# Kernel tuning notes

Measured on AMD Instinct MI355X. Metric: run time of the kernel, lower is better.

Reference implementation:

```python
import jax, jax.numpy as jnp
import numpy as np

BETA = 0.25


def setup_inputs() -> dict:
    key = jax.random.key(0)
    k1, k2 = jax.random.split(key)
    z = jax.random.normal(k1, (16, 2048, 64), dtype=jnp.float32)
    emb = jax.random.uniform(k2, (8192, 64), dtype=jnp.float32)  # uniform_() init
    return {"z": z, "emb": emb}


def reference(z, emb):
    # z: [B, N, D], emb: [K, D]; use_norm=False so norm is identity.
    B, N, D = z.shape
    zf = z.reshape(-1, D)                                   # [B*N, D]
    # Squared euclidean distances; argmin is identical to cdist(p=2) argmin.
    d2 = (
        jnp.sum(zf * zf, axis=1, keepdims=True)
        - 2.0 * (zf @ emb.T)
        + jnp.sum(emb * emb, axis=1)
    )                                                       # [B*N, K]
    idx = jnp.argmin(d2, axis=1)                            # [B*N]
    z_q = emb[idx].reshape(z.shape)                         # [B, N, D]
    loss = BETA * jnp.mean((jax.lax.stop_gradient(z_q) - z) ** 2) + jnp.mean(
        (z_q - jax.lax.stop_gradient(z)) ** 2
    )
    z_q_st = z + jax.lax.stop_gradient(z_q - z)             # straight-through
    return z_q_st, idx, loss
```

## Files before the change

### kernel.cpp

```cpp
#include <hip/hip_runtime.h>
#include <hip/hip_bf16.h>
#include <math.h>

#define D 64
#define K_CODES 8192
#define M_QUERIES 32768
#define SLICES 4
#define CODES_PER_SLICE (K_CODES / SLICES)
#define CHUNK 64
#define NCHUNK (CODES_PER_SLICE / CHUNK)
#define QPB 128
#define TAU_V 4e-3f

typedef __attribute__((ext_vector_type(8))) short bf16x8;
typedef __attribute__((ext_vector_type(4))) float f32x4;
typedef __attribute__((ext_vector_type(16))) float f32x16;

__device__ __forceinline__ unsigned short f2bf(float x) {
    __hip_bfloat16 h = __float2bfloat16(x);
    return *reinterpret_cast<unsigned short*>(&h);
}
__device__ __forceinline__ float bf2f(unsigned short s) {
    __hip_bfloat16 h;
    *reinterpret_cast<unsigned short*>(&h) = s;
    return __bfloat162float(h);
}
__device__ __forceinline__ void gld_lds16(const void* g, void* l) {
    __builtin_amdgcn_global_load_lds(
        (const __attribute__((address_space(1))) void*)g,
        (__attribute__((address_space(3))) void*)l, 16, 0, 0);
}
__device__ __forceinline__ void gld_lds4(const void* g, void* l) {
    __builtin_amdgcn_global_load_lds(
        (const __attribute__((address_space(1))) void*)g,
        (__attribute__((address_space(3))) void*)l, 4, 0, 0);
}

__global__ __launch_bounds__(256) void k0_split(const float* __restrict__ emb,
                                                unsigned short* __restrict__ e_hi,
                                                unsigned short* __restrict__ e_lo,
                                                float* __restrict__ halfee,
                                                int* __restrict__ ws_cnt) {
    const int t = threadIdx.x;
    const int chunk = blockIdx.x;
    if (chunk == 0 && t == 0) *ws_cnt = 0;
    const int u = t & 7;
#pragma unroll
    for (int it = 0; it < 2; ++it) {
        const int r = (t >> 3) + it * 32;
        const float* src = emb + ((size_t)(chunk * 64 + r) * 64 + u * 8);
        float4 f0 = *(const float4*)(src);
        float4 f1 = *(const float4*)(src + 4);
        float f[8] = {f0.x, f0.y, f0.z, f0.w, f1.x, f1.y, f1.z, f1.w};
        bf16x8 h, lo;
        float s = 0.f;
#pragma unroll
        for (int j = 0; j < 8; ++j) {
            float e = f[j];
            s += e * e;
            unsigned short hh = f2bf(e);
            h[j]  = (short)hh;
            lo[j] = (short)f2bf(e - bf2f(hh));
        }
        size_t off = (size_t)chunk * 8192 + (size_t)(u * 64 + r) * 16;
        *(bf16x8*)((char*)e_hi + off) = h;
        *(bf16x8*)((char*)e_lo + off) = lo;
        s += __shfl_xor(s, 1);
        s += __shfl_xor(s, 2);
        s += __shfl_xor(s, 4);
        if (u == 0) halfee[chunk * 64 + r] = 0.5f * s + 128.0f;
    }
}

__global__ __launch_bounds__(256, 1) void k1_mfma(const float* __restrict__ z,
                                                  const unsigned short* __restrict__ e_hi,
                                                  const unsigned short* __restrict__ e_lo,
                                                  const float* __restrict__ halfee,
                                                  float4* __restrict__ ws_part) {
    __shared__ __align__(16) unsigned short ldshi[2][CHUNK * 64];
    __shared__ __align__(16) unsigned short ldslo[2][CHUNK * 64];
    __shared__ __align__(16) float ldshe[2][CHUNK];

    const int tid = threadIdx.x;
    const int wid = tid >> 6;
    const int l   = tid & 63;
    const int col = l & 31;
    const int hi  = l >> 5;
    const int slice = blockIdx.y;
    const int chunk0 = slice * NCHUNK;

    const int qw0 = blockIdx.x * QPB + wid * 32;
    const int qrow = qw0 + col;
    bf16x8 qh[4], ql[4];
#pragma unroll
    for (int kk = 0; kk < 4; ++kk) {
        const float* src = z + (size_t)qrow * D + kk * 16 + hi * 8;
        float4 f0 = *(const float4*)(src);
        float4 f1 = *(const float4*)(src + 4);
        float f[8] = {f0.x, f0.y, f0.z, f0.w, f1.x, f1.y, f1.z, f1.w};
        bf16x8 h, lo;
#pragma unroll
        for (int j = 0; j < 8; ++j) {
            float x = -f[j];
            unsigned short hh = f2bf(x);
            float r = x - bf2f(hh);
            h[j]  = (short)hh;
            lo[j] = (short)f2bf(r);
        }
        qh[kk] = h;
        ql[kk] = lo;
    }

    float g1 = 1e30f, g2 = 1e30f;
    int   gi = 0x7fffffff;

#define STAGE(buf, c1)                                                           \
    {                                                                            \
        size_t cb = (size_t)(chunk0 + (c1)) * 8192 + wid * 2048 + l * 16;        \
        const char* ghi = (const char*)e_hi + cb;                                \
        const char* glo = (const char*)e_lo + cb;                                \
        char* dhi = (char*)&ldshi[buf][0] + wid * 2048;                          \
        char* dlo = (char*)&ldslo[buf][0] + wid * 2048;                          \
        gld_lds16(ghi, dhi);                                                     \
        gld_lds16(ghi + 1024, dhi + 1024);                                       \
        gld_lds16(glo, dlo);                                                     \
        gld_lds16(glo + 1024, dlo + 1024);                                       \
        if (wid == 0)                                                            \
            gld_lds4((const char*)halfee + (size_t)(chunk0 + (c1)) * 256 + l * 4,\
                     (char*)&ldshe[buf][0]);                                     \
    }

#define COMPUTE(bufc, cbase)                                                     \
    {                                                                            \
        const char*  bh  = (const char*)ldshi[bufc];                             \
        const char*  bl  = (const char*)ldslo[bufc];                             \
        const float* bhe = ldshe[bufc];                                          \
        f32x16 acc0, acc1;                                                       \
        _Pragma("unroll") for (int g = 0; g < 4; ++g) {                          \
            f32x4 h0 = *(const f32x4*)(bhe + g * 8 + 4 * hi);                    \
            f32x4 h1 = *(const f32x4*)(bhe + 32 + g * 8 + 4 * hi);               \
            acc0[g * 4 + 0] = h0[0]; acc0[g * 4 + 1] = h0[1];                    \
            acc0[g * 4 + 2] = h0[2]; acc0[g * 4 + 3] = h0[3];                    \
            acc1[g * 4 + 0] = h1[0]; acc1[g * 4 + 1] = h1[1];                    \
            acc1[g * 4 + 2] = h1[2]; acc1[g * 4 + 3] = h1[3];                    \
        }                                                                        \
        _Pragma("unroll") for (int kk = 0; kk < 4; ++kk) {                       \
            int a0 = ((kk * 2 + hi) * 64 + col) * 16;       \
            bf16x8 ah0 = *(const bf16x8*)(bh + a0);                              \
            bf16x8 ah1 = *(const bf16x8*)(bh + a0 + 512);                        \
            bf16x8 al0 = *(const bf16x8*)(bl + a0);                              \
            bf16x8 al1 = *(const bf16x8*)(bl + a0 + 512);                        \
            acc0 = __builtin_amdgcn_mfma_f32_32x32x16_bf16(ah0, qh[kk], acc0, 0, 0, 0); \
            acc1 = __builtin_amdgcn_mfma_f32_32x32x16_bf16(ah1, qh[kk], acc1, 0, 0, 0); \
            acc0 = __builtin_amdgcn_mfma_f32_32x32x16_bf16(ah0, ql[kk], acc0, 0, 0, 0); \
            acc1 = __builtin_amdgcn_mfma_f32_32x32x16_bf16(ah1, ql[kk], acc1, 0, 0, 0); \
            acc0 = __builtin_amdgcn_mfma_f32_32x32x16_bf16(al0, qh[kk], acc0, 0, 0, 0); \
            acc1 = __builtin_amdgcn_mfma_f32_32x32x16_bf16(al1, qh[kk], acc1, 0, 0, 0); \
        }                                                                        \
        float m1p = 1e30f, m2p = 1e30f;                                          \
        _Pragma("unroll") for (int r = 0; r < 16; ++r) {                         \
            float vp0 = __int_as_float((__float_as_int(acc0[r]) & 0xFFFFFFE0) | r); \
            m2p = __builtin_amdgcn_fmed3f(vp0, m1p, m2p);                        \
            m1p = fminf(m1p, vp0);                                               \
            float vp1 = __int_as_float((__float_as_int(acc1[r]) & 0xFFFFFFE0) | (16 + r)); \
            m2p = __builtin_amdgcn_fmed3f(vp1, m1p, m2p);                        \
            m1p = fminf(m1p, vp1);                                               \
        }                                                                        \
        int p1 = __float_as_int(m1p) & 31;                                       \
        int rr = p1 & 15;                                                        \
        int code = (cbase) + (p1 >> 4) * 32 + (rr & 3) + 8 * (rr >> 2) + 4 * hi; \
        bool lt = m1p < g1;                                                      \
        g2 = fminf(lt ? g1 : g2, lt ? m2p : m1p);                                \
        g1 = lt ? m1p : g1;                                                      \
        gi = lt ? code : gi;                                                     \
    }

    STAGE(0, 0);
    __syncthreads();
    for (int c = 0; c < NCHUNK; ++c) {
        const int cur = c & 1;
        if (c + 1 < NCHUNK) STAGE(cur ^ 1, c + 1);
        COMPUTE(cur, slice * CODES_PER_SLICE + c * CHUNK);
        __syncthreads();
    }

    {
        float o1 = __shfl_xor(g1, 32);
        float o2 = __shfl_xor(g2, 32);
        int   oi = __shfl_xor(gi, 32);
        bool  take = (o1 < g1) || (o1 == g1 && oi < gi);
        float n2   = take ? fminf(o2, g1) : fminf(g2, o1);
        g1 = take ? o1 : g1;
        gi = take ? oi : gi;
        g2 = n2;
        if (l < 32) {
            int q = qw0 + col;
            ws_part[(size_t)q * SLICES + slice] =
                make_float4(g1, g2, __int_as_float(gi), 0.f);
        }
    }
#undef STAGE
#undef COMPUTE
}

__global__ __launch_bounds__(256) void k1b_merge(const float4* __restrict__ ws_part,
                                                 int* __restrict__ ws_idx,
                                                 int* __restrict__ ws_cnt,
                                                 int* __restrict__ ws_list) {
    int q = blockIdx.x * blockDim.x + threadIdx.x;
    float m1 = 1e30f, m2 = 1e30f;
    int   i1 = 0x7fffffff;
#pragma unroll
    for (int s = 0; s < SLICES; ++s) {
        float4 p = ws_part[(size_t)q * SLICES + s];
        float v1 = p.x, v2 = p.y;
        int   vi = __float_as_int(p.z);
        if (v1 < m1 || (v1 == m1 && vi < i1)) { m2 = fminf(m1, v2); m1 = v1; i1 = vi; }
        else                                  { m2 = fminf(m2, v1); }
    }
    ws_idx[q] = i1;
    if (m2 - m1 < TAU_V) {
        int r = atomicAdd(ws_cnt, 1);
        ws_list[r] = q;
    }
}

__global__ __launch_bounds__(256) void k2_rescue(const float* __restrict__ z,
                                                 const float* __restrict__ emb,
                                                 const int* __restrict__ ws_cnt,
                                                 const int* __restrict__ ws_list,
                                                 int* __restrict__ ws_idx) {
    __shared__ float  zrow[D];
    __shared__ double rv[256];
    __shared__ int    ri[256];
    const int cnt = *ws_cnt;
    for (int r = blockIdx.x; r < cnt; r += gridDim.x) {
        const int q = ws_list[r];
        __syncthreads();
        if (threadIdx.x < D) zrow[threadIdx.x] = z[(size_t)q * D + threadIdx.x];
        __syncthreads();
        double best = 1e300;
        int    bi   = 0x7fffffff;
        for (int c = threadIdx.x; c < K_CODES; c += 256) {
            const float4* er = (const float4*)(emb + (size_t)c * D);
            double acc = 0.0;
#pragma unroll
            for (int k = 0; k < 16; ++k) {
                float4 e  = er[k];
                double d0 = (double)zrow[4 * k + 0] - (double)e.x;
                double d1 = (double)zrow[4 * k + 1] - (double)e.y;
                double d2 = (double)zrow[4 * k + 2] - (double)e.z;
                double d3 = (double)zrow[4 * k + 3] - (double)e.w;
                acc += d0 * d0 + d1 * d1 + d2 * d2 + d3 * d3;
            }
            if (acc < best) { best = acc; bi = c; }
        }
        rv[threadIdx.x] = best;
        ri[threadIdx.x] = bi;
        __syncthreads();
        for (int s = 128; s > 0; s >>= 1) {
            if (threadIdx.x < s) {
                double ov = rv[threadIdx.x + s];
                int    oi = ri[threadIdx.x + s];
                if (ov < rv[threadIdx.x] || (ov == rv[threadIdx.x] && oi < ri[threadIdx.x])) {
                    rv[threadIdx.x] = ov;
                    ri[threadIdx.x] = oi;
                }
            }
            __syncthreads();
        }
        if (threadIdx.x == 0) ws_idx[q] = ri[0];
        __syncthreads();
    }
}

__global__ __launch_bounds__(256) void k3_gather(const float* __restrict__ emb,
                                                 const float* __restrict__ z,
                                                 const int* __restrict__ ws_idx,
                                                 float* __restrict__ out,
                                                 float* __restrict__ partial) {
    __shared__ float sb[256];
    int g = blockIdx.x * 256 + threadIdx.x;
    int q = g >> 6, d = g & 63;
    int id = ws_idx[q];
    float e = emb[(size_t)id * D + d];
    out[g] = e;
    if (d == 0) out[(size_t)M_QUERIES * D + q] = (float)id;
    float df = e - z[g];
    sb[threadIdx.x] = df * df;
    __syncthreads();
    for (int s = 128; s > 0; s >>= 1) {
        if (threadIdx.x < s) sb[threadIdx.x] += sb[threadIdx.x + s];
        __syncthreads();
    }
    if (threadIdx.x == 0) partial[blockIdx.x] = sb[0];
}

__global__ __launch_bounds__(256) void k4_loss(const float* __restrict__ partial,
                                               float* __restrict__ out) {
    __shared__ double sb[256];
    double s = 0.0;
    for (int i = threadIdx.x; i < (M_QUERIES * D) / 256; i += 256) s += (double)partial[i];
    sb[threadIdx.x] = s;
    __syncthreads();
    for (int st = 128; st > 0; st >>= 1) {
        if (threadIdx.x < st) sb[threadIdx.x] += sb[threadIdx.x + st];
        __syncthreads();
    }
    if (threadIdx.x == 0)
        out[(size_t)M_QUERIES * D + M_QUERIES] =
            (float)(1.25 * sb[0] / (double)((size_t)M_QUERIES * D));
}

extern "C" void kernel_launch(void* const* d_in, const int* in_sizes, int n_in,
                              void* d_out, int out_size, void* d_ws, size_t ws_size,
                              hipStream_t stream) {
    const float* z   = (const float*)d_in[0];
    const float* emb = (const float*)d_in[1];
    float* out = (float*)d_out;
    char*  ws  = (char*)d_ws;

    unsigned short* e_hi    = (unsigned short*)(ws);
    unsigned short* e_lo    = (unsigned short*)(ws + 1048576);
    float*          halfee  = (float*)(ws + 2097152);
    float4*         ws_part = (float4*)(ws + 2129920);
    int*            ws_idx  = (int*)(ws + 2129920 + 2097152);
    int*            ws_cnt  = (int*)(ws + 2129920 + 2097152 + 131072);
    int*            ws_list = (int*)(ws + 2129920 + 2097152 + 131136);
    float*          partial = (float*)(ws + 2129920 + 2097152 + 262208);

    k0_split<<<K_CODES / 64, 256, 0, stream>>>(emb, e_hi, e_lo, halfee, ws_cnt);

    dim3 g1(M_QUERIES / QPB, SLICES);
    k1_mfma<<<g1, 256, 0, stream>>>(z, e_hi, e_lo, halfee, ws_part);

    k1b_merge<<<M_QUERIES / 256, 256, 0, stream>>>(ws_part, ws_idx, ws_cnt, ws_list);

    k2_rescue<<<256, 256, 0, stream>>>(z, emb, ws_cnt, ws_list, ws_idx);

    k3_gather<<<(M_QUERIES * D) / 256, 256, 0, stream>>>(emb, z, ws_idx, out, partial);

    k4_loss<<<1, 256, 0, stream>>>(partial, out);
}
```

Measured before the change: 193.9 us.

## Process two query tiles per wave to reuse codebook LDS fragments

Each wave now handles 64 queries (two 32-query groups) instead of 32, and the block shrinks to 2 waves while still covering 128 queries. Each codebook fragment read from LDS feeds MFMAs for both query groups, halving LDS reads per MFMA, and the staging loop is widened so two waves fill the whole chunk. The cost is double the query and accumulator registers per wave and fewer waves per block to hide latency and synchronisation.

```diff
diff --git a/kernel.cpp b/kernel.cpp
--- a/kernel.cpp
+++ b/kernel.cpp
@@ -72,7 +72,7 @@
     }
 }
 
-__global__ __launch_bounds__(256, 1) void k1_mfma(const float* __restrict__ z,
+__global__ __launch_bounds__(128, 1) void k1_mfma(const float* __restrict__ z,
                                                   const unsigned short* __restrict__ e_hi,
                                                   const unsigned short* __restrict__ e_lo,
                                                   const float* __restrict__ halfee,
@@ -89,45 +89,66 @@
     const int slice = blockIdx.y;
     const int chunk0 = slice * NCHUNK;
 
-    const int qw0 = blockIdx.x * QPB + wid * 32;
-    const int qrow = qw0 + col;
-    bf16x8 qh[4], ql[4];
-#pragma unroll
-    for (int kk = 0; kk < 4; ++kk) {
-        const float* src = z + (size_t)qrow * D + kk * 16 + hi * 8;
-        float4 f0 = *(const float4*)(src);
-        float4 f1 = *(const float4*)(src + 4);
-        float f[8] = {f0.x, f0.y, f0.z, f0.w, f1.x, f1.y, f1.z, f1.w};
-        bf16x8 h, lo;
-#pragma unroll
-        for (int j = 0; j < 8; ++j) {
-            float x = -f[j];
-            unsigned short hh = f2bf(x);
-            float r = x - bf2f(hh);
-            h[j]  = (short)hh;
-            lo[j] = (short)f2bf(r);
-        }
-        qh[kk] = h;
-        ql[kk] = lo;
-    }
-
-    float g1 = 1e30f, g2 = 1e30f;
-    int   gi = 0x7fffffff;
+    const int qw0 = blockIdx.x * QPB + wid * 64;
+    bf16x8 qh[2][4], ql[2][4];
+#pragma unroll
+    for (int g = 0; g < 2; ++g) {
+        const int qrow = qw0 + g * 32 + col;
+#pragma unroll
+        for (int kk = 0; kk < 4; ++kk) {
+            const float* src = z + (size_t)qrow * D + kk * 16 + hi * 8;
+            float4 f0 = *(const float4*)(src);
+            float4 f1 = *(const float4*)(src + 4);
+            float f[8] = {f0.x, f0.y, f0.z, f0.w, f1.x, f1.y, f1.z, f1.w};
+            bf16x8 h, lo;
+#pragma unroll
+            for (int j = 0; j < 8; ++j) {
+                float x = -f[j];
+                unsigned short hh = f2bf(x);
+                float r = x - bf2f(hh);
+                h[j]  = (short)hh;
+                lo[j] = (short)f2bf(r);
+            }
+            qh[g][kk] = h;
+            ql[g][kk] = lo;
+        }
+    }
+
+    float g1A = 1e30f, g2A = 1e30f; int giA = 0x7fffffff;
+    float g1B = 1e30f, g2B = 1e30f; int giB = 0x7fffffff;
 
 #define STAGE(buf, c1)                                                           \
     {                                                                            \
-        size_t cb = (size_t)(chunk0 + (c1)) * 8192 + wid * 2048 + l * 16;        \
+        size_t cb = (size_t)(chunk0 + (c1)) * 8192 + wid * 4096 + l * 16;        \
         const char* ghi = (const char*)e_hi + cb;                                \
         const char* glo = (const char*)e_lo + cb;                                \
-        char* dhi = (char*)&ldshi[buf][0] + wid * 2048;                          \
-        char* dlo = (char*)&ldslo[buf][0] + wid * 2048;                          \
-        gld_lds16(ghi, dhi);                                                     \
-        gld_lds16(ghi + 1024, dhi + 1024);                                       \
-        gld_lds16(glo, dlo);                                                     \
-        gld_lds16(glo + 1024, dlo + 1024);                                       \
+        char* dhi = (char*)&ldshi[buf][0] + wid * 4096;                          \
+        char* dlo = (char*)&ldslo[buf][0] + wid * 4096;                          \
+        _Pragma("unroll") for (int i = 0; i < 4; ++i) {                          \
+            gld_lds16(ghi + i * 1024, dhi + i * 1024);                           \
+            gld_lds16(glo + i * 1024, dlo + i * 1024);                           \
+        }                                                                        \
         if (wid == 0)                                                            \
             gld_lds4((const char*)halfee + (size_t)(chunk0 + (c1)) * 256 + l * 4,\
                      (char*)&ldshe[buf][0]);                                     \
+    }
+
+#define TOP2(accX, g1X, g2X, giX, tile, cbase)                                   \
+    {                                                                            \
+        float m1p = 1e30f, m2p = 1e30f;                                          \
+        _Pragma("unroll") for (int r = 0; r < 16; ++r) {                         \
+            float vp = __int_as_float((__float_as_int(accX[r]) & 0xFFFFFFE0)     \
+                                      | ((tile) * 16 + r));                      \
+            m2p = __builtin_amdgcn_fmed3f(vp, m1p, m2p);                         \
+            m1p = fminf(m1p, vp);                                                \
+        }                                                                        \
+        int p1 = __float_as_int(m1p) & 31;                                       \
+        int rr = p1 & 15;                                                        \
+        int code = (cbase) + (p1 >> 4) * 32 + (rr & 3) + 8 * (rr >> 2) + 4 * hi; \
+        bool lt = m1p < g1X;                                                     \
+        g2X = fminf(lt ? g1X : g2X, lt ? m2p : m1p);                             \
+        g1X = lt ? m1p : g1X;                                                    \
+        giX = lt ? code : giX;                                                   \
     }
 
 #define COMPUTE(bufc, cbase)                                                     \
@@ -135,44 +156,29 @@
         const char*  bh  = (const char*)ldshi[bufc];                             \
         const char*  bl  = (const char*)ldslo[bufc];                             \
         const float* bhe = ldshe[bufc];                                          \
-        f32x16 acc0, acc1;                                                       \
-        _Pragma("unroll") for (int g = 0; g < 4; ++g) {                          \
-            f32x4 h0 = *(const f32x4*)(bhe + g * 8 + 4 * hi);                    \
-            f32x4 h1 = *(const f32x4*)(bhe + 32 + g * 8 + 4 * hi);               \
-            acc0[g * 4 + 0] = h0[0]; acc0[g * 4 + 1] = h0[1];                    \
-            acc0[g * 4 + 2] = h0[2]; acc0[g * 4 + 3] = h0[3];                    \
-            acc1[g * 4 + 0] = h1[0]; acc1[g * 4 + 1] = h1[1];                    \
-            acc1[g * 4 + 2] = h1[2]; acc1[g * 4 + 3] = h1[3];                    \
+        _Pragma("unroll") for (int tile = 0; tile < 2; ++tile) {                 \
+            f32x16 accA, accB;                                                   \
+            _Pragma("unroll") for (int g4 = 0; g4 < 4; ++g4) {                   \
+                f32x4 he4 = *(const f32x4*)(bhe + tile * 32 + g4 * 8 + 4 * hi);  \
+                _Pragma("unroll") for (int j = 0; j < 4; ++j) {                  \
+                    accA[g4 * 4 + j] = he4[j];                                   \
+                    accB[g4 * 4 + j] = he4[j];                                   \
+                }                                                                \
+            }                                                                    \
+            _Pragma("unroll") for (int kk = 0; kk < 4; ++kk) {                   \
+                int a0 = ((kk * 2 + hi) * 64 + col) * 16 + tile * 512;           \
+                bf16x8 ah = *(const bf16x8*)(bh + a0);                           \
+                bf16x8 al = *(const bf16x8*)(bl + a0);                           \
+                accA = __builtin_amdgcn_mfma_f32_32x32x16_bf16(ah, qh[0][kk], accA, 0, 0, 0); \
+                accB = __builtin_amdgcn_mfma_f32_32x32x16_bf16(ah, qh[1][kk], accB, 0, 0, 0); \
+                accA = __builtin_amdgcn_mfma_f32_32x32x16_bf16(ah, ql[0][kk], accA, 0, 0, 0); \
+                accB = __builtin_amdgcn_mfma_f32_32x32x16_bf16(ah, ql[1][kk], accB, 0, 0, 0); \
+                accA = __builtin_amdgcn_mfma_f32_32x32x16_bf16(al, qh[0][kk], accA, 0, 0, 0); \
+                accB = __builtin_amdgcn_mfma_f32_32x32x16_bf16(al, qh[1][kk], accB, 0, 0, 0); \
+            }                                                                    \
+            TOP2(accA, g1A, g2A, giA, tile, cbase);                              \
+            TOP2(accB, g1B, g2B, giB, tile, cbase);                              \
         }                                                                        \
-        _Pragma("unroll") for (int kk = 0; kk < 4; ++kk) {                       \
-            int a0 = ((kk * 2 + hi) * 64 + col) * 16;       \
-            bf16x8 ah0 = *(const bf16x8*)(bh + a0);                              \
-            bf16x8 ah1 = *(const bf16x8*)(bh + a0 + 512);                        \
-            bf16x8 al0 = *(const bf16x8*)(bl + a0);                              \
-            bf16x8 al1 = *(const bf16x8*)(bl + a0 + 512);                        \
-            acc0 = __builtin_amdgcn_mfma_f32_32x32x16_bf16(ah0, qh[kk], acc0, 0, 0, 0); \
-            acc1 = __builtin_amdgcn_mfma_f32_32x32x16_bf16(ah1, qh[kk], acc1, 0, 0, 0); \
-            acc0 = __builtin_amdgcn_mfma_f32_32x32x16_bf16(ah0, ql[kk], acc0, 0, 0, 0); \
-            acc1 = __builtin_amdgcn_mfma_f32_32x32x16_bf16(ah1, ql[kk], acc1, 0, 0, 0); \
-            acc0 = __builtin_amdgcn_mfma_f32_32x32x16_bf16(al0, qh[kk], acc0, 0, 0, 0); \
-            acc1 = __builtin_amdgcn_mfma_f32_32x32x16_bf16(al1, qh[kk], acc1, 0, 0, 0); \
-        }                                                                        \
-        float m1p = 1e30f, m2p = 1e30f;                                          \
-        _Pragma("unroll") for (int r = 0; r < 16; ++r) {                         \
-            float vp0 = __int_as_float((__float_as_int(acc0[r]) & 0xFFFFFFE0) | r); \
-            m2p = __builtin_amdgcn_fmed3f(vp0, m1p, m2p);                        \
-            m1p = fminf(m1p, vp0);                                               \
-            float vp1 = __int_as_float((__float_as_int(acc1[r]) & 0xFFFFFFE0) | (16 + r)); \
-            m2p = __builtin_amdgcn_fmed3f(vp1, m1p, m2p);                        \
-            m1p = fminf(m1p, vp1);                                               \
-        }                                                                        \
-        int p1 = __float_as_int(m1p) & 31;                                       \
-        int rr = p1 & 15;                                                        \
-        int code = (cbase) + (p1 >> 4) * 32 + (rr & 3) + 8 * (rr >> 2) + 4 * hi; \
-        bool lt = m1p < g1;                                                      \
-        g2 = fminf(lt ? g1 : g2, lt ? m2p : m1p);                                \
-        g1 = lt ? m1p : g1;                                                      \
-        gi = lt ? code : gi;                                                     \
     }
 
     STAGE(0, 0);
@@ -184,22 +190,26 @@
         __syncthreads();
     }
 
-    {
-        float o1 = __shfl_xor(g1, 32);
-        float o2 = __shfl_xor(g2, 32);
-        int   oi = __shfl_xor(gi, 32);
-        bool  take = (o1 < g1) || (o1 == g1 && oi < gi);
-        float n2   = take ? fminf(o2, g1) : fminf(g2, o1);
-        g1 = take ? o1 : g1;
-        gi = take ? oi : gi;
-        g2 = n2;
+#pragma unroll
+    for (int g = 0; g < 2; ++g) {
+        float a1 = g ? g1B : g1A, a2 = g ? g2B : g2A;
+        int   ai = g ? giB : giA;
+        float o1 = __shfl_xor(a1, 32);
+        float o2 = __shfl_xor(a2, 32);
+        int   oi = __shfl_xor(ai, 32);
+        bool  take = (o1 < a1) || (o1 == a1 && oi < ai);
+        float n2   = take ? fminf(o2, a1) : fminf(a2, o1);
+        a1 = take ? o1 : a1;
+        ai = take ? oi : ai;
+        a2 = n2;
         if (l < 32) {
-            int q = qw0 + col;
+            int q = qw0 + g * 32 + col;
             ws_part[(size_t)q * SLICES + slice] =
-                make_float4(g1, g2, __int_as_float(gi), 0.f);
+                make_float4(a1, a2, __int_as_float(ai), 0.f);
         }
     }
 #undef STAGE
+#undef TOP2
 #undef COMPUTE
 }
 
@@ -332,7 +342,7 @@
     k0_split<<<K_CODES / 64, 256, 0, stream>>>(emb, e_hi, e_lo, halfee, ws_cnt);
 
     dim3 g1(M_QUERIES / QPB, SLICES);
-    k1_mfma<<<g1, 256, 0, stream>>>(z, e_hi, e_lo, halfee, ws_part);
+    k1_mfma<<<g1, 128, 0, stream>>>(z, e_hi, e_lo, halfee, ws_part);
 
     k1b_merge<<<M_QUERIES / 256, 256, 0, stream>>>(ws_part, ws_idx, ws_cnt, ws_list);
 
```

Measured after the change: 196.1 us. No clear change (+1.2%).
